# Kernel optimization log

Hardware: AMD Instinct MI355X
Metric: run time of the kernel (lower is better)

## Reference

```python
import jax, jax.numpy as jnp
import numpy as np

DMODEL = 128
HEAD = 128
SEQ = 4096
BATCH = 16

def setup_inputs() -> dict:
    key = jax.random.key(0)
    kx, kq, kk, kv = jax.random.split(key, 4)
    x = jax.random.normal(kx, (BATCH, SEQ, DMODEL), dtype=jnp.float32)
    # nn.Linear(dmodel, head_size, bias=False): store as (dmodel, head_size) so q = x @ Wq
    s = 1.0 / np.sqrt(DMODEL)
    Wq = jax.random.uniform(kq, (DMODEL, HEAD), jnp.float32, -s, s)
    Wk = jax.random.uniform(kk, (DMODEL, HEAD), jnp.float32, -s, s)
    Wv = jax.random.uniform(kv, (DMODEL, HEAD), jnp.float32, -s, s)
    return {"x": x, "Wq": Wq, "Wk": Wk, "Wv": Wv}

def reference(x, Wq, Wk, Wv):
    B, L, _ = x.shape
    scale = HEAD ** (-0.5)
    q = jnp.einsum('bld,dh->blh', x, Wq)
    k = jnp.einsum('bld,dh->blh', x, Wk)
    v = jnp.einsum('bld,dh->blh', x, Wv)
    wei = jnp.einsum('bqh,bkh->bqk', q, k) * scale  # (B, L, L)
    causal = jnp.tril(jnp.ones((L, L), dtype=bool))
    wei = jnp.where(causal, wei, -jnp.inf)
    wei = jax.nn.softmax(wei, axis=-1)
    y = jnp.einsum('bqk,bkh->bqh', wei, v)
    return y
```

## Files before the change

### kernel.cpp

```cpp
#include <hip/hip_runtime.h>
#include <hip/hip_bf16.h>
#include <stdint.h>

#define SEQ   4096
#define DM    128
#define KVB   64

typedef __attribute__((ext_vector_type(8)))  short  bf16x8;
typedef __attribute__((ext_vector_type(16))) float  f32x16;

#define SCALE_LOG2E 0.12751743f

__device__ __forceinline__ f32x16 mfma_32x32x16(bf16x8 a, bf16x8 b, f32x16 c) {
  return __builtin_amdgcn_mfma_f32_32x32x16_bf16(a, b, c, 0, 0, 0);
}

__device__ __forceinline__ void gload16(const void* g, void* l) {
  __builtin_amdgcn_global_load_lds(
      (const __attribute__((address_space(1))) unsigned int*)g,
      (__attribute__((address_space(3))) unsigned int*)l, 16, 0, 0);
}

__device__ __forceinline__ unsigned pack2bf(float a, float b) {
  float2 t; t.x = a; t.y = b;
  __hip_bfloat162 h = __float22bfloat162_rn(t);
  union { __hip_bfloat162 h2; unsigned u; } cv;
  cv.h2 = h;
  return cv.u;
}

__device__ __forceinline__ float us2f(unsigned short u) {
  union { unsigned int i; float f; } c; c.i = ((unsigned)u) << 16; return c.f;
}

__device__ __forceinline__ float fast_exp2(float x) {
#if defined(__has_builtin)
#if __has_builtin(__builtin_amdgcn_exp2f)
  return __builtin_amdgcn_exp2f(x);
#else
  return exp2f(x);
#endif
#else
  return exp2f(x);
#endif
}

__global__ void prep_w(const float* __restrict__ Wq, const float* __restrict__ Wk,
                       const float* __restrict__ Wv, __hip_bfloat16* __restrict__ Wb) {
  int t = blockIdx.x * 256 + threadIdx.x;
  if (t >= 12 * 8 * 64) return;
  int ct  = t >> 9;
  int rem = t & 511;
  int s   = rem >> 6;
  int l   = rem & 63;
  const float* W = (ct < 4) ? Wq : (ct < 8) ? Wk : Wv;
  float c = (ct < 4) ? SCALE_LOG2E : 1.0f;
  int h  = (ct & 3) * 32 + (l & 31);
  int d0 = 16 * s + 8 * (l >> 5);
  union { __hip_bfloat16 h8[8]; bf16x8 v; } u;
#pragma unroll
  for (int i = 0; i < 8; ++i) u.h8[i] = __float2bfloat16(W[(d0 + i) * DM + h] * c);
  *(bf16x8*)&Wb[(size_t)t * 8] = u.v;
}

__global__ void __launch_bounds__(256, 2)
proj(const float* __restrict__ x, const __hip_bfloat16* __restrict__ Wb,
     __hip_bfloat16* __restrict__ qw, __hip_bfloat16* __restrict__ kw,
     __hip_bfloat16* __restrict__ vtw) {
  __shared__ __hip_bfloat16 slab[4][1024];
  const int wave = threadIdx.x >> 6, lane = threadIdx.x & 63;
  const int l31 = lane & 31, hi = lane >> 5;
  const int t0 = blockIdx.x * 128 + wave * 32;
  const int trow = t0 + l31;

  bf16x8 af[8];
#pragma unroll
  for (int s = 0; s < 8; ++s) {
    const float* px = x + (size_t)trow * DM + 16 * s + 8 * hi;
    float4 u0 = *(const float4*)px;
    float4 u1 = *(const float4*)(px + 4);
    union { bf16x8 v; unsigned u[4]; } fr;
    fr.u[0] = pack2bf(u0.x, u0.y);
    fr.u[1] = pack2bf(u0.z, u0.w);
    fr.u[2] = pack2bf(u1.x, u1.y);
    fr.u[3] = pack2bf(u1.z, u1.w);
    af[s] = fr.v;
  }

  for (int ct = 0; ct < 12; ++ct) {
    f32x16 acc;
#pragma unroll
    for (int j = 0; j < 16; ++j) acc[j] = 0.f;
#pragma unroll
    for (int s = 0; s < 8; ++s) {
      bf16x8 bfr = *(const bf16x8*)&Wb[(size_t)((ct * 8 + s) * 64 + lane) * 8];
      acc = mfma_32x32x16(af[s], bfr, acc);
    }
    __syncthreads();
#pragma unroll
    for (int j = 0; j < 16; ++j) {
      int r = (j & 3) + 8 * (j >> 2) + 4 * hi;
      slab[wave][r * 32 + l31] = __float2bfloat16(acc[j]);
    }
    __syncthreads();
    if (ct < 8) {
      __hip_bfloat16* dst = (ct < 4) ? qw : kw;
      int hb = (ct & 3) * 32;
#pragma unroll
      for (int p = 0; p < 2; ++p) {
        int eidx = p * 512 + lane * 8;
        int tr = eidx >> 5, c = eidx & 31;
        *(bf16x8*)&dst[(size_t)(t0 + tr) * DM + hb + c] =
            *(const bf16x8*)&slab[wave][eidx];
      }
    } else {
      int d  = lane >> 1;
      int th = (lane & 1) * 16;
      int dg = (ct & 3) * 32 + d;
      int bb = t0 >> 12;
      int tl = t0 & 4095;
      __hip_bfloat16* dst = vtw + ((size_t)bb * DM + dg) * SEQ + tl + th;
#pragma unroll
      for (int k = 0; k < 4; ++k) {
        union { unsigned short u4[4]; uint2 v; } pkv;
#pragma unroll
        for (int e = 0; e < 4; ++e) {
          union { __hip_bfloat16 hh; unsigned short us; } cv;
          cv.hh = slab[wave][(th + 4 * k + e) * 32 + d];
          pkv.u4[e] = cv.us;
        }
        *(uint2*)&dst[4 * k] = pkv.v;
      }
    }
  }
}

__device__ __forceinline__ void stage_k(const char* kb, int tile, char* kdst,
                                        int tid, int wave) {
  const char* ksrc = kb + (size_t)tile * (KVB * 256);
#pragma unroll
  for (int p = 0; p < 4; ++p) {
    int lin = p * 4096 + tid * 16;
    int row = lin >> 8, cb = lin & 255;
    int col = cb ^ ((row & 15) << 4);
    gload16(ksrc + row * 256 + col, kdst + p * 4096 + (wave << 10));
  }
}

__device__ __forceinline__ void stage_v(const char* vb, int tile, char* vdst,
                                        int tid, int wave) {
  const char* vsrc = vb + (size_t)tile * (KVB * 2);
#pragma unroll
  for (int p = 0; p < 4; ++p) {
    int lin = p * 4096 + tid * 16;
    int row = lin >> 8, cb = lin & 255;
    int col = cb ^ ((row & 15) << 4);
    size_t so = (size_t)(2 * row + (col >> 7)) * 8192 + (size_t)(col & 127);
    gload16(vsrc + so, vdst + p * 4096 + (wave << 10));
  }
}

__global__ void __launch_bounds__(256, 2)
attn(const __hip_bfloat16* __restrict__ qw, const __hip_bfloat16* __restrict__ kw,
     const __hip_bfloat16* __restrict__ vtw, float* __restrict__ out,
     float* __restrict__ lsumA, float* __restrict__ lsumB,
     __hip_bfloat16* __restrict__ partB) {
  __shared__ __align__(16) char lds[81920];
  const int bid = blockIdx.x;
  const int b   = bid & 15;
  const int i   = (bid >> 4) & 15;
  const int isB = bid >> 8;
  const int bigQ = 31 - i;
  const int m = b * 16 + (15 - i);

  const int wave = threadIdx.x >> 6, lane = threadIdx.x & 63;
  const int l31 = lane & 31, hi = lane >> 5;
  const int tid = threadIdx.x;

  const char* kb = (const char*)(kw + (size_t)b * SEQ * DM);
  const char* vb = (const char*)(vtw + (size_t)b * DM * SEQ);

  char* k_cur = lds;         char* k_nxt = lds + 16384; char* k_nn = lds + 32768;
  char* v_cur = lds + 49152; char* v_nxt = lds + 65536;

  auto visit = [&](int qt, int t0, int cnt, int mode) {
    const int q0 = qt << 7;
    const int qrow = q0 + wave * 32 + l31;
    const int qminw = q0 + wave * 32;
    const int qmaxw = qminw + 31;

    bf16x8 qf[8];
    {
      const __hip_bfloat16* qb = qw + ((size_t)b * SEQ + qrow) * DM;
#pragma unroll
      for (int s = 0; s < 8; ++s) qf[s] = *(const bf16x8*)&qb[16 * s + 8 * hi];
    }
    f32x16 yacc[4];
#pragma unroll
    for (int dt = 0; dt < 4; ++dt)
#pragma unroll
      for (int jj = 0; jj < 16; ++jj) yacc[dt][jj] = 0.f;
    f32x16 psum;
#pragma unroll
    for (int jj = 0; jj < 16; ++jj) psum[jj] = 0.f;

    stage_k(kb, t0, k_cur, tid, wave);
    stage_v(vb, t0, v_cur, tid, wave);
    stage_k(kb, (cnt > 1 ? t0 + 1 : t0), k_nxt, tid, wave);
    __builtin_amdgcn_sched_barrier(0);
    asm volatile("s_waitcnt vmcnt(4)" ::: "memory");
    __builtin_amdgcn_s_barrier();
    __builtin_amdgcn_sched_barrier(0);

    for (int u = 0; u < cnt; ++u) {
      const int t  = t0 + u;
      const int uv = (u + 1 < cnt) ? u + 1 : cnt - 1;
      const int uk = (u + 2 < cnt) ? u + 2 : cnt - 1;
      stage_v(vb, t0 + uv, v_nxt, tid, wave);
      stage_k(kb, t0 + uk, k_nn, tid, wave);

      const int kv0 = t * KVB;
      if (kv0 <= qmaxw) {
        f32x16 sa, sb;
#pragma unroll
        for (int jj = 0; jj < 16; ++jj) { sa[jj] = 0.f; sb[jj] = 0.f; }
        __builtin_amdgcn_s_setprio(1);
#pragma unroll
        for (int s = 0; s < 8; ++s) {
          int cbs = 32 * s + 16 * hi;
          int r0 = l31, r1 = l31 + 32;
          bf16x8 k0 = *(const bf16x8*)&k_cur[r0 * 256 + (cbs ^ ((r0 & 15) << 4))];
          bf16x8 k1 = *(const bf16x8*)&k_cur[r1 * 256 + (cbs ^ ((r1 & 15) << 4))];
          sa = mfma_32x32x16(k0, qf[s], sa);
          sb = mfma_32x32x16(k1, qf[s], sb);
        }
        __builtin_amdgcn_s_setprio(0);
        if (kv0 + 63 > qminw) {
#pragma unroll
          for (int jj = 0; jj < 16; ++jj) {
            int rr = (jj & 3) + 8 * (jj >> 2) + 4 * hi;
            sa[jj] = (kv0 + rr      > qrow) ? -1e30f : sa[jj];
            sb[jj] = (kv0 + 32 + rr > qrow) ? -1e30f : sb[jj];
          }
        }
#pragma unroll
        for (int jj = 0; jj < 16; ++jj) sa[jj] = fast_exp2(sa[jj]);
#pragma unroll
        for (int jj = 0; jj < 16; ++jj) sb[jj] = fast_exp2(sb[jj]);
#pragma unroll
        for (int jj = 0; jj < 16; ++jj) psum[jj] += sa[jj] + sb[jj];

#pragma unroll
        for (int a = 0; a < 2; ++a) {
          unsigned pk[8];
#pragma unroll
          for (int jj = 0; jj < 8; ++jj) {
            float lo  = a ? sb[2 * jj]     : sa[2 * jj];
            float hi2 = a ? sb[2 * jj + 1] : sa[2 * jj + 1];
            pk[jj] = pack2bf(lo, hi2);
          }
#pragma unroll
          for (int s2 = 0; s2 < 2; ++s2) {
            int base = 4 * s2;
            unsigned a0 = pk[base + 0], b0 = pk[base + 2];
            unsigned a1 = pk[base + 1], b1 = pk[base + 3];
            asm volatile("v_permlane32_swap_b32 %0, %1" : "+v"(a0), "+v"(b0));
            asm volatile("v_permlane32_swap_b32 %0, %1" : "+v"(a1), "+v"(b1));
            union { bf16x8 v; unsigned u[4]; } pf;
            pf.u[0] = a0;
            pf.u[1] = a1;
            pf.u[2] = b0;
            pf.u[3] = b1;
            __builtin_amdgcn_s_setprio(1);
#pragma unroll
            for (int dt = 0; dt < 4; ++dt) {
              int vrow = (l31 >> 1) + 16 * dt;
              int vcol = (l31 & 1) * 128 + 64 * a + 32 * s2 + 16 * hi;
              bf16x8 vf = *(const bf16x8*)&v_cur[vrow * 256 +
                                                 (vcol ^ ((vrow & 15) << 4))];
              yacc[dt] = mfma_32x32x16(vf, pf.v, yacc[dt]);
            }
            __builtin_amdgcn_s_setprio(0);
          }
        }
      }
      __builtin_amdgcn_sched_barrier(0);
      asm volatile("s_waitcnt vmcnt(4)" ::: "memory");
      __builtin_amdgcn_s_barrier();
      __builtin_amdgcn_sched_barrier(0);
      char* tmp = k_cur; k_cur = k_nxt; k_nxt = k_nn; k_nn = tmp;
      tmp = v_cur; v_cur = v_nxt; v_nxt = tmp;
    }
    __builtin_amdgcn_sched_barrier(0);
    asm volatile("s_waitcnt vmcnt(0)" ::: "memory");
    __builtin_amdgcn_s_barrier();
    __builtin_amdgcn_sched_barrier(0);

    float lsum = 0.f;
#pragma unroll
    for (int jj = 0; jj < 16; ++jj) lsum += psum[jj];
    lsum += __shfl_xor(lsum, 32);

    float* ob = out + ((size_t)b * SEQ + qrow) * DM;
    if (mode == 0) {
      float inv = 1.0f / lsum;
#pragma unroll
      for (int dt = 0; dt < 4; ++dt) {
#pragma unroll
        for (int g = 0; g < 4; ++g) {
          float4 v;
          v.x = yacc[dt][4 * g + 0] * inv;
          v.y = yacc[dt][4 * g + 1] * inv;
          v.z = yacc[dt][4 * g + 2] * inv;
          v.w = yacc[dt][4 * g + 3] * inv;
          *(float4*)&ob[32 * dt + 8 * g + 4 * hi] = v;
        }
      }
    } else if (mode == 1) {
#pragma unroll
      for (int dt = 0; dt < 4; ++dt) {
#pragma unroll
        for (int g = 0; g < 4; ++g) {
          float4 v;
          v.x = yacc[dt][4 * g + 0];
          v.y = yacc[dt][4 * g + 1];
          v.z = yacc[dt][4 * g + 2];
          v.w = yacc[dt][4 * g + 3];
          *(float4*)&ob[32 * dt + 8 * g + 4 * hi] = v;
        }
      }
      if (hi == 0) lsumA[m * 128 + wave * 32 + l31] = lsum;
    } else {
      __hip_bfloat16* pb = partB + ((size_t)m * 128 + wave * 32 + l31) * DM;
#pragma unroll
      for (int dt = 0; dt < 4; ++dt) {
#pragma unroll
        for (int g = 0; g < 4; ++g) {
          uint2 pv;
          pv.x = pack2bf(yacc[dt][4 * g + 0], yacc[dt][4 * g + 1]);
          pv.y = pack2bf(yacc[dt][4 * g + 2], yacc[dt][4 * g + 3]);
          *(uint2*)&pb[32 * dt + 8 * g + 4 * hi] = pv;
        }
      }
      if (hi == 0) lsumB[m * 128 + wave * 32 + l31] = lsum;
    }
  };

  if (!isB) {
    visit(bigQ, 0, 33, 1);
  } else {
    visit(bigQ, 33, 31 - 2 * i, 2);
    visit(i, 0, 2 * i + 2, 0);
  }
}

__global__ void __launch_bounds__(256)
merge(float* __restrict__ out, const float* __restrict__ lsumA,
      const float* __restrict__ lsumB, const __hip_bfloat16* __restrict__ partB) {
  __shared__ float invls[128];
  const int m = blockIdx.x;
  const int b = m >> 4;
  const int Q = 16 + (m & 15);
  const int tid = threadIdx.x;
  if (tid < 128) invls[tid] = 1.0f / (lsumA[m * 128 + tid] + lsumB[m * 128 + tid]);
  __syncthreads();
  float4* o4 = (float4*)(out + ((size_t)b * SEQ + (size_t)Q * 128) * DM);
  const __hip_bfloat16* pb = partB + (size_t)m * 128 * DM;
#pragma unroll
  for (int k = 0; k < 16; ++k) {
    int e4 = tid + 256 * k;
    int row = e4 >> 5;
    float4 a = o4[e4];
    union { uint2 v; unsigned short s[4]; } pv;
    pv.v = *(const uint2*)&pb[e4 * 4];
    float inv = invls[row];
    float4 r;
    r.x = (a.x + us2f(pv.s[0])) * inv;
    r.y = (a.y + us2f(pv.s[1])) * inv;
    r.z = (a.z + us2f(pv.s[2])) * inv;
    r.w = (a.w + us2f(pv.s[3])) * inv;
    o4[e4] = r;
  }
}

extern "C" void kernel_launch(void* const* d_in, const int* in_sizes, int n_in,
                              void* d_out, int out_size, void* d_ws, size_t ws_size,
                              hipStream_t stream) {
  const float* x  = (const float*)d_in[0];
  const float* Wq = (const float*)d_in[1];
  const float* Wk = (const float*)d_in[2];
  const float* Wv = (const float*)d_in[3];
  float* out = (float*)d_out;

  char* ws = (char*)d_ws;
  __hip_bfloat16* qw    = (__hip_bfloat16*)(ws);
  __hip_bfloat16* kw    = (__hip_bfloat16*)(ws + (size_t)16 * 1024 * 1024);
  __hip_bfloat16* vtw   = (__hip_bfloat16*)(ws + (size_t)32 * 1024 * 1024);
  __hip_bfloat16* Wb    = (__hip_bfloat16*)(ws + (size_t)48 * 1024 * 1024);
  float*          lsumA = (float*)(ws + (size_t)48 * 1024 * 1024 + 128 * 1024);
  float*          lsumB = (float*)(ws + (size_t)48 * 1024 * 1024 + 256 * 1024);
  __hip_bfloat16* partB = (__hip_bfloat16*)(ws + (size_t)48 * 1024 * 1024 + 384 * 1024);

  prep_w<<<24, 256, 0, stream>>>(Wq, Wk, Wv, Wb);
  proj<<<512, 256, 0, stream>>>(x, Wb, qw, kw, vtw);
  attn<<<512, 256, 0, stream>>>(qw, kw, vtw, out, lsumA, lsumB, partB);
  merge<<<256, 256, 0, stream>>>(out, lsumA, lsumB, partB);
}
```

Baseline: 124.5 us.

## Enlarge attention Q tile to 256 rows with 8-wave blocks and XCD-aware mapping

```diff
diff --git a/kernel.cpp b/kernel.cpp
--- a/kernel.cpp
+++ b/kernel.cpp
@@ -139,11 +139,11 @@
                                         int tid, int wave) {
   const char* ksrc = kb + (size_t)tile * (KVB * 256);
 #pragma unroll
-  for (int p = 0; p < 4; ++p) {
-    int lin = p * 4096 + tid * 16;
+  for (int p = 0; p < 2; ++p) {
+    int lin = p * 8192 + tid * 16;
     int row = lin >> 8, cb = lin & 255;
     int col = cb ^ ((row & 15) << 4);
-    gload16(ksrc + row * 256 + col, kdst + p * 4096 + (wave << 10));
+    gload16(ksrc + row * 256 + col, kdst + p * 8192 + (wave << 10));
   }
 }
 
@@ -151,27 +151,30 @@
                                         int tid, int wave) {
   const char* vsrc = vb + (size_t)tile * (KVB * 2);
 #pragma unroll
-  for (int p = 0; p < 4; ++p) {
-    int lin = p * 4096 + tid * 16;
+  for (int p = 0; p < 2; ++p) {
+    int lin = p * 8192 + tid * 16;
     int row = lin >> 8, cb = lin & 255;
     int col = cb ^ ((row & 15) << 4);
     size_t so = (size_t)(2 * row + (col >> 7)) * 8192 + (size_t)(col & 127);
-    gload16(vsrc + so, vdst + p * 4096 + (wave << 10));
-  }
-}
-
-__global__ void __launch_bounds__(256, 2)
+    gload16(vsrc + so, vdst + p * 8192 + (wave << 10));
+  }
+}
+
+__global__ void __launch_bounds__(512, 2)
 attn(const __hip_bfloat16* __restrict__ qw, const __hip_bfloat16* __restrict__ kw,
      const __hip_bfloat16* __restrict__ vtw, float* __restrict__ out,
      float* __restrict__ lsumA, float* __restrict__ lsumB,
      __hip_bfloat16* __restrict__ partB) {
   __shared__ __align__(16) char lds[81920];
   const int bid = blockIdx.x;
-  const int b   = bid & 15;
-  const int i   = (bid >> 4) & 15;
-  const int isB = bid >> 8;
-  const int bigQ = 31 - i;
-  const int m = b * 16 + (15 - i);
+  const int xcd = bid & 7;
+  const int g   = bid >> 3;
+  const int b   = xcd + 8 * (g & 1);
+  const int j16 = g >> 1;
+  const int i   = j16 & 7;
+  const int isB = j16 >> 3;
+  const int bigQ = 15 - i;
+  const int m = b * 8 + i;
 
   const int wave = threadIdx.x >> 6, lane = threadIdx.x & 63;
   const int l31 = lane & 31, hi = lane >> 5;
@@ -184,7 +187,7 @@
   char* v_cur = lds + 49152; char* v_nxt = lds + 65536;
 
   auto visit = [&](int qt, int t0, int cnt, int mode) {
-    const int q0 = qt << 7;
+    const int q0 = qt << 8;
     const int qrow = q0 + wave * 32 + l31;
     const int qminw = q0 + wave * 32;
     const int qmaxw = qminw + 31;
@@ -208,7 +211,7 @@
     stage_v(vb, t0, v_cur, tid, wave);
     stage_k(kb, (cnt > 1 ? t0 + 1 : t0), k_nxt, tid, wave);
     __builtin_amdgcn_sched_barrier(0);
-    asm volatile("s_waitcnt vmcnt(4)" ::: "memory");
+    asm volatile("s_waitcnt vmcnt(2)" ::: "memory");
     __builtin_amdgcn_s_barrier();
     __builtin_amdgcn_sched_barrier(0);
 
@@ -285,7 +288,7 @@
         }
       }
       __builtin_amdgcn_sched_barrier(0);
-      asm volatile("s_waitcnt vmcnt(4)" ::: "memory");
+      asm volatile("s_waitcnt vmcnt(2)" ::: "memory");
       __builtin_amdgcn_s_barrier();
       __builtin_amdgcn_sched_barrier(0);
       char* tmp = k_cur; k_cur = k_nxt; k_nxt = k_nn; k_nn = tmp;
@@ -302,72 +305,73 @@
     lsum += __shfl_xor(lsum, 32);
 
     float* ob = out + ((size_t)b * SEQ + qrow) * DM;
+    const int row = wave * 32 + l31;
     if (mode == 0) {
       float inv = 1.0f / lsum;
 #pragma unroll
       for (int dt = 0; dt < 4; ++dt) {
 #pragma unroll
-        for (int g = 0; g < 4; ++g) {
+        for (int g2 = 0; g2 < 4; ++g2) {
           float4 v;
-          v.x = yacc[dt][4 * g + 0] * inv;
-          v.y = yacc[dt][4 * g + 1] * inv;
-          v.z = yacc[dt][4 * g + 2] * inv;
-          v.w = yacc[dt][4 * g + 3] * inv;
-          *(float4*)&ob[32 * dt + 8 * g + 4 * hi] = v;
+          v.x = yacc[dt][4 * g2 + 0] * inv;
+          v.y = yacc[dt][4 * g2 + 1] * inv;
+          v.z = yacc[dt][4 * g2 + 2] * inv;
+          v.w = yacc[dt][4 * g2 + 3] * inv;
+          *(float4*)&ob[32 * dt + 8 * g2 + 4 * hi] = v;
         }
       }
     } else if (mode == 1) {
 #pragma unroll
       for (int dt = 0; dt < 4; ++dt) {
 #pragma unroll
-        for (int g = 0; g < 4; ++g) {
+        for (int g2 = 0; g2 < 4; ++g2) {
           float4 v;
-          v.x = yacc[dt][4 * g + 0];
-          v.y = yacc[dt][4 * g + 1];
-          v.z = yacc[dt][4 * g + 2];
-          v.w = yacc[dt][4 * g + 3];
-          *(float4*)&ob[32 * dt + 8 * g + 4 * hi] = v;
-        }
-      }
-      if (hi == 0) lsumA[m * 128 + wave * 32 + l31] = lsum;
+          v.x = yacc[dt][4 * g2 + 0];
+          v.y = yacc[dt][4 * g2 + 1];
+          v.z = yacc[dt][4 * g2 + 2];
+          v.w = yacc[dt][4 * g2 + 3];
+          *(float4*)&ob[32 * dt + 8 * g2 + 4 * hi] = v;
+        }
+      }
+      if (hi == 0) lsumA[m * 256 + row] = lsum;
     } else {
-      __hip_bfloat16* pb = partB + ((size_t)m * 128 + wave * 32 + l31) * DM;
+      __hip_bfloat16* pb = partB + ((size_t)m * 256 + row) * DM;
 #pragma unroll
       for (int dt = 0; dt < 4; ++dt) {
 #pragma unroll
-        for (int g = 0; g < 4; ++g) {
+        for (int g2 = 0; g2 < 4; ++g2) {
           uint2 pv;
-          pv.x = pack2bf(yacc[dt][4 * g + 0], yacc[dt][4 * g + 1]);
-          pv.y = pack2bf(yacc[dt][4 * g + 2], yacc[dt][4 * g + 3]);
-          *(uint2*)&pb[32 * dt + 8 * g + 4 * hi] = pv;
-        }
-      }
-      if (hi == 0) lsumB[m * 128 + wave * 32 + l31] = lsum;
+          pv.x = pack2bf(yacc[dt][4 * g2 + 0], yacc[dt][4 * g2 + 1]);
+          pv.y = pack2bf(yacc[dt][4 * g2 + 2], yacc[dt][4 * g2 + 3]);
+          *(uint2*)&pb[32 * dt + 8 * g2 + 4 * hi] = pv;
+        }
+      }
+      if (hi == 0) lsumB[m * 256 + row] = lsum;
     }
   };
 
   if (!isB) {
-    visit(bigQ, 0, 33, 1);
+    visit(bigQ, 0, 34, 1);
   } else {
-    visit(bigQ, 33, 31 - 2 * i, 2);
-    visit(i, 0, 2 * i + 2, 0);
+    visit(bigQ, 34, 30 - 4 * i, 2);
+    visit(i, 0, 4 * i + 4, 0);
   }
 }
 
 __global__ void __launch_bounds__(256)
 merge(float* __restrict__ out, const float* __restrict__ lsumA,
       const float* __restrict__ lsumB, const __hip_bfloat16* __restrict__ partB) {
-  __shared__ float invls[128];
+  __shared__ float invls[256];
   const int m = blockIdx.x;
-  const int b = m >> 4;
-  const int Q = 16 + (m & 15);
+  const int b = m >> 3;
+  const int Q = 15 - (m & 7);
   const int tid = threadIdx.x;
-  if (tid < 128) invls[tid] = 1.0f / (lsumA[m * 128 + tid] + lsumB[m * 128 + tid]);
+  invls[tid] = 1.0f / (lsumA[m * 256 + tid] + lsumB[m * 256 + tid]);
   __syncthreads();
-  float4* o4 = (float4*)(out + ((size_t)b * SEQ + (size_t)Q * 128) * DM);
-  const __hip_bfloat16* pb = partB + (size_t)m * 128 * DM;
-#pragma unroll
-  for (int k = 0; k < 16; ++k) {
+  float4* o4 = (float4*)(out + ((size_t)b * SEQ + (size_t)Q * 256) * DM);
+  const __hip_bfloat16* pb = partB + (size_t)m * 256 * DM;
+#pragma unroll
+  for (int k = 0; k < 32; ++k) {
     int e4 = tid + 256 * k;
     int row = e4 >> 5;
     float4 a = o4[e4];
@@ -403,6 +407,6 @@
 
   prep_w<<<24, 256, 0, stream>>>(Wq, Wk, Wv, Wb);
   proj<<<512, 256, 0, stream>>>(x, Wb, qw, kw, vtw);
-  attn<<<512, 256, 0, stream>>>(qw, kw, vtw, out, lsumA, lsumB, partB);
-  merge<<<256, 256, 0, stream>>>(out, lsumA, lsumB, partB);
-}
+  attn<<<256, 512, 0, stream>>>(qw, kw, vtw, out, lsumA, lsumB, partB);
+  merge<<<128, 256, 0, stream>>>(out, lsumA, lsumB, partB);
+}
```

After: 120.8 us. 1.03x faster.
